# Optimization experiments

Hardware: AMD Instinct MI355X
Metric: run time of the kernel (lower is better)

## Reference

```python
import jax, jax.numpy as jnp
import numpy as np

H, W, C = 96, 96, 21
THETA_ALPHA, THETA_BETA, THETA_GAMMA = 8.0, 0.125, 3.0
NUM_ITERATIONS = 5


def setup_inputs() -> dict:
    key = jax.random.key(0)
    k1, k2, k3, k4, k5 = jax.random.split(key, 5)
    unaries = jax.random.normal(k1, (1, H, W, C), dtype=jnp.float32)
    reference_image = jax.random.uniform(k2, (1, H, W, 3), dtype=jnp.float32)
    # truncated normal(mean=0, std=0.1) as in tf.initializers.truncated_normal
    spatial_ker_weights = 0.1 * jax.random.truncated_normal(k3, -2.0, 2.0, (C,), dtype=jnp.float32)
    bilateral_ker_weights = 0.1 * jax.random.truncated_normal(k4, -2.0, 2.0, (C,), dtype=jnp.float32)
    compatibility_matrix = 0.1 * jax.random.truncated_normal(k5, -2.0, 2.0, (C, C), dtype=jnp.float32)
    return {
        "unaries": unaries,
        "reference_image": reference_image,
        "spatial_ker_weights": spatial_ker_weights,
        "bilateral_ker_weights": bilateral_ker_weights,
        "compatibility_matrix": compatibility_matrix,
    }


def _gaussian_kernel(feats):
    # feats: [B, N, D] -> K[b, i, j] = exp(-0.5 * ||f_i - f_j||^2)
    sq = jnp.sum(feats * feats, axis=-1)  # [B, N]
    d2 = sq[:, :, None] + sq[:, None, :] - 2.0 * jnp.einsum("bnd,bmd->bnm", feats, feats)
    return jnp.exp(-0.5 * jnp.maximum(d2, 0.0))


def _build_kernels(reference_image):
    # Exact-math equivalent of the permutohedral lattice Gaussian filter:
    # spatial features = positions/theta_gamma; bilateral = [pos/theta_alpha, rgb/theta_beta].
    B = reference_image.shape[0]
    yy, xx = jnp.meshgrid(jnp.arange(H, dtype=jnp.float32), jnp.arange(W, dtype=jnp.float32), indexing="ij")
    pos = jnp.stack([yy, xx], axis=-1).reshape(1, H * W, 2)  # [1, N, 2]
    pos = jnp.broadcast_to(pos, (B, H * W, 2))
    col = reference_image.reshape(B, H * W, 3)
    k_spatial = _gaussian_kernel(pos / THETA_GAMMA)
    k_bilateral = _gaussian_kernel(jnp.concatenate([pos / THETA_ALPHA, col / THETA_BETA], axis=-1))
    return k_spatial, k_bilateral


def reference(unaries, reference_image, spatial_ker_weights, bilateral_ker_weights, compatibility_matrix):
    B = unaries.shape[0]
    N = H * W
    k_spatial, k_bilateral = _build_kernels(reference_image)  # built once; reused each iteration
    u = unaries.reshape(B, N, C)
    q = u
    for _ in range(NUM_ITERATIONS):
        q = jax.nn.softmax(q, axis=-1)
        spatial_out = jnp.einsum("bnm,bmc->bnc", k_spatial, q)
        bilateral_out = jnp.einsum("bnm,bmc->bnc", k_bilateral, q)
        # pairwise^T = compat @ diag(w_s) @ S^T + compat @ diag(w_b) @ Bi^T
        # => pairwise = (S * w_s + Bi * w_b) @ compat^T
        message = spatial_out * spatial_ker_weights + bilateral_out * bilateral_ker_weights
        pairwise = message @ compatibility_matrix.T
        q = u - pairwise
    return q.reshape(unaries.shape)
```

## Files before the change

### kernel.cpp

```cpp
#include <hip/hip_runtime.h>
#include <hip/hip_bf16.h>

#define HH 96
#define WW 96
#define CC 21
#define NN (HH*WW)
#define NELEM (NN*CC)
#define RS 20
#define NPAR (2*CC + CC*CC)
#define L2E 1.4426950408889634f
#define NMC 48
#define NBB (36*NMC)
#define NBLUR (CC*8)
#define SROWS 12
#define TRUNC2 900
#define BLURKEY 0x10000

typedef short bf16x8 __attribute__((ext_vector_type(8)));
typedef float f32x16 __attribute__((ext_vector_type(16)));

__device__ __forceinline__ float fexp2(float x) { return __builtin_amdgcn_exp2f(x); }
__device__ __forceinline__ float fexp(float x)  { return __builtin_amdgcn_exp2f(x * L2E); }

__device__ __forceinline__ short f2b(float f) {
    __hip_bfloat16 h = __float2bfloat16(f);
    short s; __builtin_memcpy(&s, &h, 2); return s;
}

struct Tab { int n; int k[NBB + NBLUR]; };
constexpr Tab build_tab() {
    Tab t{};
    int key[NBB + NBLUR] = {};
    int cst[NBB + NBLUR] = {};
    int m = 0;
    for (int nt = 0; nt < 36; nt++)
        for (int mc = 0; mc < NMC; mc++) {
            const int ny0 = (nt / 6) * 16, nx0 = (nt % 6) * 16;
            const int my0 = (mc & 7) * 12, mx0 = (mc >> 3) * 16;
            const int dx = (mx0 > nx0 + 15) ? mx0 - (nx0 + 15)
                         : ((nx0 > mx0 + 15) ? nx0 - (mx0 + 15) : 0);
            const int lim = TRUNC2 - dx * dx;
            if (lim < 0) continue;
            int T = 0;
            while ((T + 1) * (T + 1) <= lim) T++;
            int cost = 0;
            for (int wv = 0; wv < 4; wv++) {
                const int by0 = ny0 + 4 * wv;
                int lo = by0 - T - my0;     if (lo < 0)  lo = 0;
                int hi = by0 + 3 + T - my0; if (hi > 11) hi = 11;
                if (lo <= hi) cost += hi - lo + 1;
            }
            if (cost == 0) continue;
            key[m] = (nt << 6) | mc; cst[m] = cost; m++;
        }
    for (int b = 0; b < NBLUR; b++) { key[m] = BLURKEY + b; cst[m] = 20; m++; }
    for (int c = 48; c >= 1; c--)
        for (int i = 0; i < m; i++)
            if (cst[i] == c) t.k[t.n++] = key[i];
    return t;
}
constexpr Tab TT = build_tab();
__device__ __constant__ Tab c_TT = TT;

__global__ void k_sniff(const unsigned short* __restrict__ u16, int* __restrict__ flag32) {
    __shared__ int sfound;
    if (threadIdx.x == 0) sfound = 0;
    __syncthreads();
    const int base = blockIdx.x * (NELEM/32);
    int found = 0;
    for (int i = base + threadIdx.x; i < base + NELEM/32; i += 256) {
        unsigned v = u16[i];
        if ((v & 0x7F80u) == 0x7F80u) found = 1;
    }
    if (found) sfound = 1;
    __syncthreads();
    if (threadIdx.x == 0) flag32[blockIdx.x] = sfound;
}

__device__ __forceinline__ int rdflag(const int* __restrict__ flag32) {
    int f = 0;
    #pragma unroll
    for (int i = 0; i < 32; i++) f |= flag32[i];
    return f;
}

__global__ __launch_bounds__(256) void k_prep(
    const void* __restrict__ u, const void* __restrict__ img,
    const void* __restrict__ wS, const void* __restrict__ wB,
    const void* __restrict__ compat, const int* __restrict__ flag32,
    float* __restrict__ uf, float* __restrict__ featx, float* __restrict__ par,
    float* __restrict__ bil, __hip_bfloat16* __restrict__ pT)
{
    const int f = rdflag(flag32);
    const int tid = threadIdx.x;
    const int n = blockIdx.x * 256 + tid;

    if (blockIdx.x == 0) {
        for (int i = tid; i < NPAR; i += 256) {
            const void* src; int j;
            if (i < CC)        { src = wS;     j = i; }
            else if (i < 2*CC) { src = wB;     j = i - CC; }
            else               { src = compat; j = i - 2*CC; }
            par[i] = f ? ((const float*)src)[j]
                       : __bfloat162float(((const __hip_bfloat16*)src)[j]);
        }
    }

    {
        float c0, c1, c2;
        if (f) { const float* p = (const float*)img;
                 c0 = p[3*n]; c1 = p[3*n+1]; c2 = p[3*n+2]; }
        else   { const __hip_bfloat16* p = (const __hip_bfloat16*)img;
                 c0 = __bfloat162float(p[3*n]); c1 = __bfloat162float(p[3*n+1]);
                 c2 = __bfloat162float(p[3*n+2]); }
        float ym = (float)(n / WW), xm = (float)(n % WW);
        const float sc = 0.15014029f;
        const float cf = 9.6089787f;
        featx[8*n + 0] = -L2E * (fmaf(ym, ym, xm*xm) * 0.0078125f
                                 + 32.f * (c0*c0 + c1*c1 + c2*c2));
        featx[8*n + 1] = sc * ym;
        featx[8*n + 2] = sc * xm;
        featx[8*n + 3] = cf * c0;
        featx[8*n + 4] = cf * c1;
        featx[8*n + 5] = cf * c2;
        featx[8*n + 6] = 0.f;
        featx[8*n + 7] = 0.f;
    }

    float v[CC];
    float mx = -1e30f;
    #pragma unroll
    for (int c = 0; c < CC; c++) {
        float uv = f ? ((const float*)u)[n*CC + c]
                     : __bfloat162float(((const __hip_bfloat16*)u)[n*CC + c]);
        uf[n*CC + c] = uv;
        v[c] = uv;
        mx = fmaxf(mx, uv);
    }
    float s = 0.f;
    #pragma unroll
    for (int c = 0; c < CC; c++) { v[c] = fexp(v[c] - mx); s += v[c]; }
    float inv = 1.f / s;
    #pragma unroll
    for (int c = 0; c < CC; c++) {
        pT[(size_t)c*NN + n] = __float2bfloat16(v[c] * inv);
        bil[(size_t)c*NN + n] = 0.f;
    }
}

__global__ __launch_bounds__(256, 4) void k_work(
    const __hip_bfloat16* __restrict__ pT,
    const float* __restrict__ featx,
    float* __restrict__ bil,
    float* __restrict__ s2T)
{
    __shared__ float smem[6176];
    const int tid = threadIdx.x;
    const int item = c_TT.k[blockIdx.x];

    if (item < BLURKEY) {
        float* lds_h = smem;
        const int wv   = tid >> 6, lane = tid & 63;
        const int quad = lane >> 5, lid = lane & 31;

        const int nt = item >> 6, mc = item & 63;
        const int ny0 = (nt / 6) * 16, nx0 = (nt % 6) * 16;
        const int my0 = (mc & 7) * 12, mx0 = (mc >> 3) * 16;

        const int dx = (mx0 > nx0 + 15) ? mx0 - (nx0 + 15)
                     : ((nx0 > mx0 + 15) ? nx0 - (mx0 + 15) : 0);
        const int lim = TRUNC2 - dx * dx;
        int T = (int)sqrtf((float)lim);
        T -= (T * T > lim);
        T += ((T + 1) * (T + 1) <= lim);

        int blo = ny0 - T - my0;      blo = blo < 0 ? 0 : blo;
        int bhi = ny0 + 15 + T - my0; bhi = bhi > 11 ? 11 : bhi;

        {
            float4* dst = (float4*)lds_h;
            for (int i = blo * 32 + tid; i < (bhi + 1) * 32; i += 256) {
                const int seg = i >> 5, off = i & 31;
                dst[i] = ((const float4*)(featx +
                          (size_t)((my0 + seg) * WW + mx0) * 8))[off];
            }
        }
        __syncthreads();

        const int by0 = ny0 + 4 * wv;
        int lo = by0 - T - my0;     lo = lo < 0 ? 0 : lo;
        int hi = by0 + 3 + T - my0; hi = hi > 11 ? 11 : hi;
        if (lo > hi) return;

        const int row = lid >> 4, col = lid & 15;
        const int n0 = (by0 + row) * WW + nx0 + col;
        const int n1 = n0 + 2 * WW;
        const float4 g0a = *(const float4*)(featx + (size_t)n0 * 8);
        const float4 g0b = *(const float4*)(featx + (size_t)n0 * 8 + 4);
        const float4 g1a = *(const float4*)(featx + (size_t)n1 * 8);
        const float4 g1b = *(const float4*)(featx + (size_t)n1 * 8 + 4);

        f32x16 acc0, acc1;
        #pragma unroll
        for (int r = 0; r < 16; r++) { acc0[r] = 0.f; acc1[r] = 0.f; }

        int mg = (my0 + lo) * WW + mx0 + quad * 8;
        for (int step = lo; step <= hi; step++, mg += WW) {
            bf16x8 afrag = *(const bf16x8*)(pT + (size_t)lid * NN + mg);

            const float* h = lds_h + (step * 16 + quad * 8) * 8;
            float kb0[8], kb1[8];
            #pragma unroll
            for (int j = 0; j < 8; j++) {
                float4 ha = *(const float4*)(h + j * 8);
                float4 hb = *(const float4*)(h + j * 8 + 4);
                float s0 = g0a.x + ha.x;
                s0 = fmaf(g0a.y, ha.y, s0);
                s0 = fmaf(g0a.z, ha.z, s0);
                s0 = fmaf(g0a.w, ha.w, s0);
                s0 = fmaf(g0b.x, hb.x, s0);
                s0 = fmaf(g0b.y, hb.y, s0);
                kb0[j] = fexp2(s0);
                float s1 = g1a.x + ha.x;
                s1 = fmaf(g1a.y, ha.y, s1);
                s1 = fmaf(g1a.z, ha.z, s1);
                s1 = fmaf(g1a.w, ha.w, s1);
                s1 = fmaf(g1b.x, hb.x, s1);
                s1 = fmaf(g1b.y, hb.y, s1);
                kb1[j] = fexp2(s1);
            }
            bf16x8 b0, b1;
            #pragma unroll
            for (int j = 0; j < 8; j++) { b0[j] = f2b(kb0[j]); b1[j] = f2b(kb1[j]); }

            acc0 = __builtin_amdgcn_mfma_f32_32x32x16_bf16(afrag, b0, acc0, 0, 0, 0);
            acc1 = __builtin_amdgcn_mfma_f32_32x32x16_bf16(afrag, b1, acc1, 0, 0, 0);
        }

        #pragma unroll
        for (int r = 0; r < 16; r++) {
            int c = (r & 3) + 8 * (r >> 2) + 4 * quad;
            if (c < CC) {
                atomicAdd(&bil[(size_t)c * NN + n0], acc0[r]);
                atomicAdd(&bil[(size_t)c * NN + n1], acc1[r]);
            }
        }
    } else {
        float* A   = smem;
        float* B2  = smem + 4992;
        float* w_s = smem + 6144;
        const int b2 = item - BLURKEY;
        const int c = b2 % CC;
        const int strip = b2 / CC;
        const int y0 = strip * SROWS;
        const int ylo = (y0 - RS < 0) ? 0 : y0 - RS;
        const int yhi = (y0 + SROWS - 1 + RS > HH - 1) ? HH - 1 : y0 + SROWS - 1 + RS;
        const int nrows = yhi - ylo + 1;

        if (tid <= RS) w_s[tid] = fexp2(-(float)(tid*tid) * (L2E / 18.f));
        const __hip_bfloat16* src = pT + (size_t)c * NN + ylo * WW;
        for (int i = tid; i < nrows * WW; i += 256)
            A[i] = __bfloat162float(src[i]);
        __syncthreads();

        for (int i = tid; i < SROWS * WW; i += 256) {
            const int yo = y0 + i / WW;
            const int x  = i % WW;
            float acc = A[(yo - ylo) * WW + x];
            #pragma unroll
            for (int d = 1; d <= RS; d++) {
                float s = 0.f;
                if (yo - d >= 0)  s += A[(yo - d - ylo) * WW + x];
                if (yo + d < HH)  s += A[(yo + d - ylo) * WW + x];
                acc = fmaf(w_s[d], s, acc);
            }
            B2[i] = acc;
        }
        __syncthreads();

        for (int i = tid; i < SROWS * WW; i += 256) {
            const int r = i / WW, x = i % WW;
            float acc = B2[i];
            #pragma unroll
            for (int d = 1; d <= RS; d++) {
                float s = 0.f;
                if (x - d >= 0)  s += B2[r * WW + x - d];
                if (x + d < WW)  s += B2[r * WW + x + d];
                acc = fmaf(w_s[d], s, acc);
            }
            s2T[(size_t)c * NN + (y0 + r) * WW + x] = acc;
        }
    }
}

__global__ __launch_bounds__(256) void k_update(
    float* __restrict__ bil, const float* __restrict__ s2T,
    const float* __restrict__ uf, const float* __restrict__ par,
    const int* __restrict__ flag32,
    __hip_bfloat16* __restrict__ pT, void* __restrict__ out, int last)
{
    __shared__ float sc[CC*CC + 1];
    __shared__ float sws[CC], swb[CC];
    const int tid = threadIdx.x;
    for (int i = tid; i < CC*CC; i += 256) sc[i] = par[2*CC + i];
    if (tid == 0) sc[CC*CC] = 0.f;
    if (tid < CC) { sws[tid] = par[tid]; swb[tid] = par[CC + tid]; }
    __syncthreads();

    const int half = tid & 1;
    const int n = blockIdx.x * 128 + (tid >> 1);

    float msg[11];
    #pragma unroll
    for (int k = 0; k < 11; k++) {
        const int cp = 2*k + half;
        if (cp < CC) {
            msg[k] = fmaf(s2T[(size_t)cp*NN + n], sws[cp],
                          bil[(size_t)cp*NN + n] * swb[cp]);
            bil[(size_t)cp*NN + n] = 0.f;
        } else msg[k] = 0.f;
    }

    float pw[CC];
    #pragma unroll
    for (int c = 0; c < CC; c++) {
        float a = msg[0] * sc[c*CC + half];
        #pragma unroll
        for (int k = 1; k < 11; k++)
            a = fmaf(msg[k], sc[c*CC + 2*k + half], a);
        pw[c] = a;
    }
    #pragma unroll
    for (int c = 0; c < CC; c++)
        pw[c] += __shfl_xor(pw[c], 1, 64);

    float qv[CC];
    float mx = -1e30f;
    #pragma unroll
    for (int c = 0; c < CC; c++) {
        qv[c] = uf[(size_t)n*CC + c] - pw[c];
        mx = fmaxf(mx, qv[c]);
    }

    if (last) {
        const int is_f32 = rdflag(flag32);
        #pragma unroll
        for (int k = 0; k < 11; k++) {
            const int ce = 2*k, co = (k < 10) ? 2*k + 1 : 0;
            float v = half ? qv[co] : qv[ce];
            const int c = 2*k + half;
            if (c < CC) {
                if (is_f32) ((float*)out)[(size_t)n*CC + c] = v;
                else ((__hip_bfloat16*)out)[(size_t)n*CC + c] = __float2bfloat16(v);
            }
        }
    } else {
        float ex[11]; float ssum = 0.f;
        #pragma unroll
        for (int k = 0; k < 11; k++) {
            const int ce = 2*k, co = (k < 10) ? 2*k + 1 : 0;
            float v = half ? qv[co] : qv[ce];
            float e = fexp(v - mx);
            if (2*k + half < CC) ssum += e;
            ex[k] = e;
        }
        ssum += __shfl_xor(ssum, 1, 64);
        const float inv = 1.f / ssum;
        #pragma unroll
        for (int k = 0; k < 11; k++) {
            const int c = 2*k + half;
            if (c < CC) pT[(size_t)c*NN + n] = __float2bfloat16(ex[k] * inv);
        }
    }
}

extern "C" void kernel_launch(void* const* d_in, const int* in_sizes, int n_in,
                              void* d_out, int out_size, void* d_ws, size_t ws_size,
                              hipStream_t stream)
{
    float* ws = (float*)d_ws;
    int*   flag32 = (int*)ws;
    float* par    = ws + 32;
    float* featx  = ws + 544;
    __hip_bfloat16* pT = (__hip_bfloat16*)(ws + 74272);
    float* uf  = ws + 221728;
    float* s2T = uf + NELEM;
    float* bil = s2T + NELEM;

    k_sniff<<<32, 256, 0, stream>>>((const unsigned short*)d_in[0], flag32);
    k_prep<<<NN/256, 256, 0, stream>>>(d_in[0], d_in[1], d_in[2], d_in[3], d_in[4],
                                       flag32, uf, featx, par, bil, pT);

    for (int it = 0; it < 5; it++) {
        k_work<<<TT.n, 256, 0, stream>>>(pT, featx, bil, s2T);
        k_update<<<NN/128, 256, 0, stream>>>(bil, s2T, uf, par, flag32,
                                             pT, d_out, (it == 4) ? 1 : 0);
    }
}
```

Before: 231.1 us.

## Fuse update into work kernel via per-tile completion counters and double-buffered probabilities

Removes the separate k_update launch. Each work block bumps an atomic counter for the output tile(s) it contributed to, and the block that finishes a tile last runs the compatibility transform, softmax and output write for that tile. Probabilities are double-buffered so the next iteration's values can be written while other blocks still read the current ones. This saves five kernel launches and their tail gaps. In exchange it adds threadfences, atomics and serial tail work in the last-arriving blocks, and drops the occupancy hint from launch_bounds.

Result: slower. 645.9 us (+179.5%).

```diff
diff --git a/kernel.cpp b/kernel.cpp
--- a/kernel.cpp
+++ b/kernel.cpp
@@ -27,12 +27,13 @@
     short s; __builtin_memcpy(&s, &h, 2); return s;
 }
 
-struct Tab { int n; int k[NBB + NBLUR]; };
+struct Tab { int n; int k[NBB + NBLUR]; int expct[36]; };
 constexpr Tab build_tab() {
     Tab t{};
     int key[NBB + NBLUR] = {};
     int cst[NBB + NBLUR] = {};
     int m = 0;
+    for (int nt = 0; nt < 36; nt++) t.expct[nt] = 42;
     for (int nt = 0; nt < 36; nt++)
         for (int mc = 0; mc < NMC; mc++) {
             const int ny0 = (nt / 6) * 16, nx0 = (nt % 6) * 16;
@@ -52,6 +53,7 @@
             }
             if (cost == 0) continue;
             key[m] = (nt << 6) | mc; cst[m] = cost; m++;
+            t.expct[nt]++;
         }
     for (int b = 0; b < NBLUR; b++) { key[m] = BLURKEY + b; cst[m] = 20; m++; }
     for (int c = 48; c >= 1; c--)
@@ -89,13 +91,14 @@
     const void* __restrict__ wS, const void* __restrict__ wB,
     const void* __restrict__ compat, const int* __restrict__ flag32,
     float* __restrict__ uf, float* __restrict__ featx, float* __restrict__ par,
-    float* __restrict__ bil, __hip_bfloat16* __restrict__ pT)
+    float* __restrict__ bil, __hip_bfloat16* __restrict__ pT, int* __restrict__ cnt)
 {
     const int f = rdflag(flag32);
     const int tid = threadIdx.x;
     const int n = blockIdx.x * 256 + tid;
 
     if (blockIdx.x == 0) {
+        if (tid < 36) cnt[tid] = 0;
         for (int i = tid; i < NPAR; i += 256) {
             const void* src; int j;
             if (i < CC)        { src = wS;     j = i; }
@@ -148,15 +151,21 @@
     }
 }
 
-__global__ __launch_bounds__(256, 4) void k_work(
-    const __hip_bfloat16* __restrict__ pT,
+__global__ __launch_bounds__(256) void k_work(
+    const __hip_bfloat16* __restrict__ pTcur,
+    __hip_bfloat16* __restrict__ pTnxt,
     const float* __restrict__ featx,
     float* __restrict__ bil,
-    float* __restrict__ s2T)
+    float* __restrict__ s2T,
+    const float* __restrict__ uf, const float* __restrict__ par,
+    const int* __restrict__ flag32, int* __restrict__ cnt,
+    void* __restrict__ out, int last)
 {
     __shared__ float smem[6176];
+    __shared__ int fin[13];
     const int tid = threadIdx.x;
     const int item = c_TT.k[blockIdx.x];
+    if (tid == 0) fin[0] = 0;
 
     if (item < BLURKEY) {
         float* lds_h = smem;
@@ -190,61 +199,70 @@
         const int by0 = ny0 + 4 * wv;
         int lo = by0 - T - my0;     lo = lo < 0 ? 0 : lo;
         int hi = by0 + 3 + T - my0; hi = hi > 11 ? 11 : hi;
-        if (lo > hi) return;
-
-        const int row = lid >> 4, col = lid & 15;
-        const int n0 = (by0 + row) * WW + nx0 + col;
-        const int n1 = n0 + 2 * WW;
-        const float4 g0a = *(const float4*)(featx + (size_t)n0 * 8);
-        const float4 g0b = *(const float4*)(featx + (size_t)n0 * 8 + 4);
-        const float4 g1a = *(const float4*)(featx + (size_t)n1 * 8);
-        const float4 g1b = *(const float4*)(featx + (size_t)n1 * 8 + 4);
-
-        f32x16 acc0, acc1;
-        #pragma unroll
-        for (int r = 0; r < 16; r++) { acc0[r] = 0.f; acc1[r] = 0.f; }
-
-        int mg = (my0 + lo) * WW + mx0 + quad * 8;
-        for (int step = lo; step <= hi; step++, mg += WW) {
-            bf16x8 afrag = *(const bf16x8*)(pT + (size_t)lid * NN + mg);
-
-            const float* h = lds_h + (step * 16 + quad * 8) * 8;
-            float kb0[8], kb1[8];
-            #pragma unroll
-            for (int j = 0; j < 8; j++) {
-                float4 ha = *(const float4*)(h + j * 8);
-                float4 hb = *(const float4*)(h + j * 8 + 4);
-                float s0 = g0a.x + ha.x;
-                s0 = fmaf(g0a.y, ha.y, s0);
-                s0 = fmaf(g0a.z, ha.z, s0);
-                s0 = fmaf(g0a.w, ha.w, s0);
-                s0 = fmaf(g0b.x, hb.x, s0);
-                s0 = fmaf(g0b.y, hb.y, s0);
-                kb0[j] = fexp2(s0);
-                float s1 = g1a.x + ha.x;
-                s1 = fmaf(g1a.y, ha.y, s1);
-                s1 = fmaf(g1a.z, ha.z, s1);
-                s1 = fmaf(g1a.w, ha.w, s1);
-                s1 = fmaf(g1b.x, hb.x, s1);
-                s1 = fmaf(g1b.y, hb.y, s1);
-                kb1[j] = fexp2(s1);
-            }
-            bf16x8 b0, b1;
-            #pragma unroll
-            for (int j = 0; j < 8; j++) { b0[j] = f2b(kb0[j]); b1[j] = f2b(kb1[j]); }
-
-            acc0 = __builtin_amdgcn_mfma_f32_32x32x16_bf16(afrag, b0, acc0, 0, 0, 0);
-            acc1 = __builtin_amdgcn_mfma_f32_32x32x16_bf16(afrag, b1, acc1, 0, 0, 0);
-        }
-
-        #pragma unroll
-        for (int r = 0; r < 16; r++) {
-            int c = (r & 3) + 8 * (r >> 2) + 4 * quad;
-            if (c < CC) {
-                atomicAdd(&bil[(size_t)c * NN + n0], acc0[r]);
-                atomicAdd(&bil[(size_t)c * NN + n1], acc1[r]);
-            }
-        }
+
+        if (lo <= hi) {
+            const int row = lid >> 4, col = lid & 15;
+            const int n0 = (by0 + row) * WW + nx0 + col;
+            const int n1 = n0 + 2 * WW;
+            const float4 g0a = *(const float4*)(featx + (size_t)n0 * 8);
+            const float4 g0b = *(const float4*)(featx + (size_t)n0 * 8 + 4);
+            const float4 g1a = *(const float4*)(featx + (size_t)n1 * 8);
+            const float4 g1b = *(const float4*)(featx + (size_t)n1 * 8 + 4);
+
+            f32x16 acc0, acc1;
+            #pragma unroll
+            for (int r = 0; r < 16; r++) { acc0[r] = 0.f; acc1[r] = 0.f; }
+
+            int mg = (my0 + lo) * WW + mx0 + quad * 8;
+            for (int step = lo; step <= hi; step++, mg += WW) {
+                bf16x8 afrag = *(const bf16x8*)(pTcur + (size_t)lid * NN + mg);
+
+                const float* h = lds_h + (step * 16 + quad * 8) * 8;
+                float kb0[8], kb1[8];
+                #pragma unroll
+                for (int j = 0; j < 8; j++) {
+                    float4 ha = *(const float4*)(h + j * 8);
+                    float4 hb = *(const float4*)(h + j * 8 + 4);
+                    float s0 = g0a.x + ha.x;
+                    s0 = fmaf(g0a.y, ha.y, s0);
+                    s0 = fmaf(g0a.z, ha.z, s0);
+                    s0 = fmaf(g0a.w, ha.w, s0);
+                    s0 = fmaf(g0b.x, hb.x, s0);
+                    s0 = fmaf(g0b.y, hb.y, s0);
+                    kb0[j] = fexp2(s0);
+                    float s1 = g1a.x + ha.x;
+                    s1 = fmaf(g1a.y, ha.y, s1);
+                    s1 = fmaf(g1a.z, ha.z, s1);
+                    s1 = fmaf(g1a.w, ha.w, s1);
+                    s1 = fmaf(g1b.x, hb.x, s1);
+                    s1 = fmaf(g1b.y, hb.y, s1);
+                    kb1[j] = fexp2(s1);
+                }
+                bf16x8 b0, b1;
+                #pragma unroll
+                for (int j = 0; j < 8; j++) { b0[j] = f2b(kb0[j]); b1[j] = f2b(kb1[j]); }
+
+                acc0 = __builtin_amdgcn_mfma_f32_32x32x16_bf16(afrag, b0, acc0, 0, 0, 0);
+                acc1 = __builtin_amdgcn_mfma_f32_32x32x16_bf16(afrag, b1, acc1, 0, 0, 0);
+            }
+
+            #pragma unroll
+            for (int r = 0; r < 16; r++) {
+                int c = (r & 3) + 8 * (r >> 2) + 4 * quad;
+                if (c < CC) {
+                    atomicAdd(&bil[(size_t)c * NN + n0], acc0[r]);
+                    atomicAdd(&bil[(size_t)c * NN + n1], acc1[r]);
+                }
+            }
+        }
+
+        __threadfence();
+        __syncthreads();
+        if (tid == 0) {
+            int old = atomicAdd(&cnt[nt], 1);
+            if (old == c_TT.expct[nt] - 1) { fin[0] = 1; fin[1] = nt; }
+        }
+        __syncthreads();
     } else {
         float* A   = smem;
         float* B2  = smem + 4992;
@@ -258,7 +276,7 @@
         const int nrows = yhi - ylo + 1;
 
         if (tid <= RS) w_s[tid] = fexp2(-(float)(tid*tid) * (L2E / 18.f));
-        const __hip_bfloat16* src = pT + (size_t)c * NN + ylo * WW;
+        const __hip_bfloat16* src = pTcur + (size_t)c * NN + ylo * WW;
         for (int i = tid; i < nrows * WW; i += 256)
             A[i] = __bfloat162float(src[i]);
         __syncthreads();
@@ -290,87 +308,76 @@
             }
             s2T[(size_t)c * NN + (y0 + r) * WW + x] = acc;
         }
-    }
-}
-
-__global__ __launch_bounds__(256) void k_update(
-    float* __restrict__ bil, const float* __restrict__ s2T,
-    const float* __restrict__ uf, const float* __restrict__ par,
-    const int* __restrict__ flag32,
-    __hip_bfloat16* __restrict__ pT, void* __restrict__ out, int last)
-{
-    __shared__ float sc[CC*CC + 1];
-    __shared__ float sws[CC], swb[CC];
-    const int tid = threadIdx.x;
+
+        __threadfence();
+        __syncthreads();
+        if (tid == 0) {
+            int nf = 0;
+            const int r0 = (12 * strip) / 16;
+            int r1 = (12 * strip + 11) / 16; if (r1 > 5) r1 = 5;
+            for (int r = r0; r <= r1; r++)
+                for (int xt = 0; xt < 6; xt++) {
+                    const int nt2 = r * 6 + xt;
+                    int old = atomicAdd(&cnt[nt2], 1);
+                    if (old == c_TT.expct[nt2] - 1) fin[1 + nf++] = nt2;
+                }
+            fin[0] = nf;
+        }
+        __syncthreads();
+    }
+
+    const int nf = fin[0];
+    if (nf == 0) return;
+    __threadfence();
+
+    float* sc  = smem;
+    float* sws = smem + 448;
+    float* swb = smem + 480;
     for (int i = tid; i < CC*CC; i += 256) sc[i] = par[2*CC + i];
-    if (tid == 0) sc[CC*CC] = 0.f;
     if (tid < CC) { sws[tid] = par[tid]; swb[tid] = par[CC + tid]; }
     __syncthreads();
 
-    const int half = tid & 1;
-    const int n = blockIdx.x * 128 + (tid >> 1);
-
-    float msg[11];
-    #pragma unroll
-    for (int k = 0; k < 11; k++) {
-        const int cp = 2*k + half;
-        if (cp < CC) {
-            msg[k] = fmaf(s2T[(size_t)cp*NN + n], sws[cp],
-                          bil[(size_t)cp*NN + n] * swb[cp]);
-            bil[(size_t)cp*NN + n] = 0.f;
-        } else msg[k] = 0.f;
-    }
-
-    float pw[CC];
-    #pragma unroll
-    for (int c = 0; c < CC; c++) {
-        float a = msg[0] * sc[c*CC + half];
+    const int is_f32 = last ? rdflag(flag32) : 0;
+
+    for (int t = 0; t < nf; t++) {
+        const int nt2 = fin[1 + t];
+        const int n = ((nt2 / 6) * 16 + (tid >> 4)) * WW + (nt2 % 6) * 16 + (tid & 15);
+
+        float msg[CC];
         #pragma unroll
-        for (int k = 1; k < 11; k++)
-            a = fmaf(msg[k], sc[c*CC + 2*k + half], a);
-        pw[c] = a;
-    }
-    #pragma unroll
-    for (int c = 0; c < CC; c++)
-        pw[c] += __shfl_xor(pw[c], 1, 64);
-
-    float qv[CC];
-    float mx = -1e30f;
-    #pragma unroll
-    for (int c = 0; c < CC; c++) {
-        qv[c] = uf[(size_t)n*CC + c] - pw[c];
-        mx = fmaxf(mx, qv[c]);
-    }
-
-    if (last) {
-        const int is_f32 = rdflag(flag32);
+        for (int c = 0; c < CC; c++) {
+            msg[c] = fmaf(s2T[(size_t)c*NN + n], sws[c],
+                          bil[(size_t)c*NN + n] * swb[c]);
+            bil[(size_t)c*NN + n] = 0.f;
+        }
+
+        float qv[CC];
+        float mx = -1e30f;
         #pragma unroll
-        for (int k = 0; k < 11; k++) {
-            const int ce = 2*k, co = (k < 10) ? 2*k + 1 : 0;
-            float v = half ? qv[co] : qv[ce];
-            const int c = 2*k + half;
-            if (c < CC) {
-                if (is_f32) ((float*)out)[(size_t)n*CC + c] = v;
-                else ((__hip_bfloat16*)out)[(size_t)n*CC + c] = __float2bfloat16(v);
-            }
-        }
-    } else {
-        float ex[11]; float ssum = 0.f;
-        #pragma unroll
-        for (int k = 0; k < 11; k++) {
-            const int ce = 2*k, co = (k < 10) ? 2*k + 1 : 0;
-            float v = half ? qv[co] : qv[ce];
-            float e = fexp(v - mx);
-            if (2*k + half < CC) ssum += e;
-            ex[k] = e;
-        }
-        ssum += __shfl_xor(ssum, 1, 64);
-        const float inv = 1.f / ssum;
-        #pragma unroll
-        for (int k = 0; k < 11; k++) {
-            const int c = 2*k + half;
-            if (c < CC) pT[(size_t)c*NN + n] = __float2bfloat16(ex[k] * inv);
-        }
+        for (int c = 0; c < CC; c++) {
+            float pw = 0.f;
+            #pragma unroll
+            for (int cp = 0; cp < CC; cp++) pw = fmaf(msg[cp], sc[c*CC + cp], pw);
+            qv[c] = uf[(size_t)n*CC + c] - pw;
+            mx = fmaxf(mx, qv[c]);
+        }
+
+        if (last) {
+            #pragma unroll
+            for (int c = 0; c < CC; c++) {
+                if (is_f32) ((float*)out)[(size_t)n*CC + c] = qv[c];
+                else ((__hip_bfloat16*)out)[(size_t)n*CC + c] = __float2bfloat16(qv[c]);
+            }
+        } else {
+            float s = 0.f;
+            #pragma unroll
+            for (int c = 0; c < CC; c++) { qv[c] = fexp(qv[c] - mx); s += qv[c]; }
+            float inv = 1.f / s;
+            #pragma unroll
+            for (int c = 0; c < CC; c++)
+                pTnxt[(size_t)c*NN + n] = __float2bfloat16(qv[c] * inv);
+        }
+        if (tid == 0) cnt[nt2] = 0;
     }
 }
 
@@ -382,18 +389,21 @@
     int*   flag32 = (int*)ws;
     float* par    = ws + 32;
     float* featx  = ws + 544;
-    __hip_bfloat16* pT = (__hip_bfloat16*)(ws + 74272);
-    float* uf  = ws + 221728;
+    __hip_bfloat16* pT0 = (__hip_bfloat16*)(ws + 74272);
+    __hip_bfloat16* pT1 = (__hip_bfloat16*)(ws + 221728);
+    float* uf  = ws + 369184;
     float* s2T = uf + NELEM;
     float* bil = s2T + NELEM;
+    int*   cnt = (int*)(bil + NELEM);
 
     k_sniff<<<32, 256, 0, stream>>>((const unsigned short*)d_in[0], flag32);
     k_prep<<<NN/256, 256, 0, stream>>>(d_in[0], d_in[1], d_in[2], d_in[3], d_in[4],
-                                       flag32, uf, featx, par, bil, pT);
+                                       flag32, uf, featx, par, bil, pT0, cnt);
 
     for (int it = 0; it < 5; it++) {
-        k_work<<<TT.n, 256, 0, stream>>>(pT, featx, bil, s2T);
-        k_update<<<NN/128, 256, 0, stream>>>(bil, s2T, uf, par, flag32,
-                                             pT, d_out, (it == 4) ? 1 : 0);
-    }
-}
+        __hip_bfloat16* cur = (it & 1) ? pT1 : pT0;
+        __hip_bfloat16* nxt = (it & 1) ? pT0 : pT1;
+        k_work<<<TT.n, 256, 0, stream>>>(cur, nxt, featx, bil, s2T, uf, par,
+                                         flag32, cnt, d_out, (it == 4) ? 1 : 0);
+    }
+}
```

## Compute bilateral kernel exponent via split-bf16 MFMA instead of scalar FMAs

Applied to the files above, without the earlier changes.

Moves the per-pair dot product of bilateral features from scalar FMA chains onto MFMA instructions. Features are split into bf16 hi/lo pairs to keep accuracy, and the exp'd results are repacked with cross-half shuffles into B fragments for the P^T·K MFMA. The block's feature strip is staged into LDS as bf16 hi/lo, processing two rows per step. It also drops the occupancy hint from launch_bounds. The trade is extra MFMAs, shuffles and register pressure, plus some precision loss from the bf16 split, in exchange for fewer VALU ops.

New measurement: 235.6 us. About the same (+2.0%).

```diff
diff --git a/kernel.cpp b/kernel.cpp
--- a/kernel.cpp
+++ b/kernel.cpp
@@ -18,6 +18,7 @@
 
 typedef short bf16x8 __attribute__((ext_vector_type(8)));
 typedef float f32x16 __attribute__((ext_vector_type(16)));
+typedef int   i32x4  __attribute__((ext_vector_type(4)));
 
 __device__ __forceinline__ float fexp2(float x) { return __builtin_amdgcn_exp2f(x); }
 __device__ __forceinline__ float fexp(float x)  { return __builtin_amdgcn_exp2f(x * L2E); }
@@ -25,6 +26,10 @@
 __device__ __forceinline__ short f2b(float f) {
     __hip_bfloat16 h = __float2bfloat16(f);
     short s; __builtin_memcpy(&s, &h, 2); return s;
+}
+__device__ __forceinline__ float b2f(short s) {
+    __hip_bfloat16 h; __builtin_memcpy(&h, &s, 2);
+    return __bfloat162float(h);
 }
 
 struct Tab { int n; int k[NBB + NBLUR]; };
@@ -148,7 +153,7 @@
     }
 }
 
-__global__ __launch_bounds__(256, 4) void k_work(
+__global__ __launch_bounds__(256) void k_work(
     const __hip_bfloat16* __restrict__ pT,
     const float* __restrict__ featx,
     float* __restrict__ bil,
@@ -159,7 +164,7 @@
     const int item = c_TT.k[blockIdx.x];
 
     if (item < BLURKEY) {
-        float* lds_h = smem;
+        short* hs = (short*)smem;
         const int wv   = tid >> 6, lane = tid & 63;
         const int quad = lane >> 5, lid = lane & 31;
 
@@ -174,15 +179,18 @@
         T -= (T * T > lim);
         T += ((T + 1) * (T + 1) <= lim);
 
-        int blo = ny0 - T - my0;      blo = blo < 0 ? 0 : blo;
-        int bhi = ny0 + 15 + T - my0; bhi = bhi > 11 ? 11 : bhi;
-
-        {
-            float4* dst = (float4*)lds_h;
-            for (int i = blo * 32 + tid; i < (bhi + 1) * 32; i += 256) {
-                const int seg = i >> 5, off = i & 31;
-                dst[i] = ((const float4*)(featx +
-                          (size_t)((my0 + seg) * WW + mx0) * 8))[off];
+        for (int i = tid; i < 192; i += 256) {
+            const int mrow = i >> 4, mcol = i & 15;
+            const float* f = featx + (size_t)((my0 + mrow) * WW + mx0 + mcol) * 8;
+            const int grp = mrow >> 1;
+            const int li  = ((mrow & 1) << 4) | mcol;
+            short* dhi = hs + grp * 512 + li * 8;
+            float hv[8] = {1.f, f[0], f[1], f[2], f[3], f[4], f[5], 0.f};
+            #pragma unroll
+            for (int j = 0; j < 8; j++) {
+                short hb = f2b(hv[j]);
+                dhi[j] = hb;
+                dhi[256 + j] = f2b(hv[j] - b2f(hb));
             }
         }
         __syncthreads();
@@ -195,46 +203,82 @@
         const int row = lid >> 4, col = lid & 15;
         const int n0 = (by0 + row) * WW + nx0 + col;
         const int n1 = n0 + 2 * WW;
-        const float4 g0a = *(const float4*)(featx + (size_t)n0 * 8);
-        const float4 g0b = *(const float4*)(featx + (size_t)n0 * 8 + 4);
-        const float4 g1a = *(const float4*)(featx + (size_t)n1 * 8);
-        const float4 g1b = *(const float4*)(featx + (size_t)n1 * 8 + 4);
-
-        f32x16 acc0, acc1;
-        #pragma unroll
-        for (int r = 0; r < 16; r++) { acc0[r] = 0.f; acc1[r] = 0.f; }
-
-        int mg = (my0 + lo) * WW + mx0 + quad * 8;
-        for (int step = lo; step <= hi; step++, mg += WW) {
-            bf16x8 afrag = *(const bf16x8*)(pT + (size_t)lid * NN + mg);
-
-            const float* h = lds_h + (step * 16 + quad * 8) * 8;
-            float kb0[8], kb1[8];
+
+        bf16x8 gh0, gl0, gh1, gl1;
+        {
+            const float* f0 = featx + (size_t)n0 * 8;
+            const float* f1 = featx + (size_t)n1 * 8;
+            float g0v[8] = {f0[0], 1.f, f0[1], f0[2], f0[3], f0[4], f0[5], 0.f};
+            float g1v[8] = {f1[0], 1.f, f1[1], f1[2], f1[3], f1[4], f1[5], 0.f};
             #pragma unroll
             for (int j = 0; j < 8; j++) {
-                float4 ha = *(const float4*)(h + j * 8);
-                float4 hb = *(const float4*)(h + j * 8 + 4);
-                float s0 = g0a.x + ha.x;
-                s0 = fmaf(g0a.y, ha.y, s0);
-                s0 = fmaf(g0a.z, ha.z, s0);
-                s0 = fmaf(g0a.w, ha.w, s0);
-                s0 = fmaf(g0b.x, hb.x, s0);
-                s0 = fmaf(g0b.y, hb.y, s0);
-                kb0[j] = fexp2(s0);
-                float s1 = g1a.x + ha.x;
-                s1 = fmaf(g1a.y, ha.y, s1);
-                s1 = fmaf(g1a.z, ha.z, s1);
-                s1 = fmaf(g1a.w, ha.w, s1);
-                s1 = fmaf(g1b.x, hb.x, s1);
-                s1 = fmaf(g1b.y, hb.y, s1);
-                kb1[j] = fexp2(s1);
-            }
-            bf16x8 b0, b1;
-            #pragma unroll
-            for (int j = 0; j < 8; j++) { b0[j] = f2b(kb0[j]); b1[j] = f2b(kb1[j]); }
-
-            acc0 = __builtin_amdgcn_mfma_f32_32x32x16_bf16(afrag, b0, acc0, 0, 0, 0);
-            acc1 = __builtin_amdgcn_mfma_f32_32x32x16_bf16(afrag, b1, acc1, 0, 0, 0);
+                short h0b = f2b(g0v[j]); gh0[j] = h0b;
+                gl0[j] = f2b(g0v[j] - b2f(h0b));
+                short h1b = f2b(g1v[j]); gh1[j] = h1b;
+                gl1[j] = f2b(g1v[j] - b2f(h1b));
+            }
+        }
+
+        f32x16 acc0, acc1, zz;
+        #pragma unroll
+        for (int r = 0; r < 16; r++) { acc0[r] = 0.f; acc1[r] = 0.f; zz[r] = 0.f; }
+
+        const int glo2 = lo >> 1, ghi2 = hi >> 1;
+        for (int g = glo2; g <= ghi2; g++) {
+            bf16x8 A1 = *(const bf16x8*)(hs + g * 512 + quad * 256 + lid * 8);
+            const int mrow = my0 + 2 * g;
+            const __hip_bfloat16* pbase = pT + (size_t)lid * NN + mrow * WW + mx0 + quad * 8;
+            bf16x8 afA = *(const bf16x8*)(pbase);
+            bf16x8 afB = *(const bf16x8*)(pbase + WW);
+
+            {
+                f32x16 V = __builtin_amdgcn_mfma_f32_32x32x16_bf16(A1, gh0, zz, 0, 0, 0);
+                V = __builtin_amdgcn_mfma_f32_32x32x16_bf16(A1, gl0, V, 0, 0, 0);
+                #pragma unroll
+                for (int r = 0; r < 16; r++) V[r] = fexp2(V[r]);
+                int P[8];
+                #pragma unroll
+                for (int t2 = 0; t2 < 8; t2++)
+                    P[t2] = (int)(((unsigned)(unsigned short)f2b(V[2*t2]))
+                          | (((unsigned)(unsigned short)f2b(V[2*t2+1])) << 16));
+                int S0 = __shfl_xor(P[0], 32), S1 = __shfl_xor(P[1], 32);
+                int S2 = __shfl_xor(P[2], 32), S3 = __shfl_xor(P[3], 32);
+                int S4 = __shfl_xor(P[4], 32), S5 = __shfl_xor(P[5], 32);
+                int S6 = __shfl_xor(P[6], 32), S7 = __shfl_xor(P[7], 32);
+                i32x4 b1i = { quad ? S2 : P[0], quad ? S3 : P[1],
+                              quad ? P[2] : S0, quad ? P[3] : S1 };
+                i32x4 b2i = { quad ? S6 : P[4], quad ? S7 : P[5],
+                              quad ? P[6] : S4, quad ? P[7] : S5 };
+                bf16x8 b1, b2;
+                __builtin_memcpy(&b1, &b1i, 16);
+                __builtin_memcpy(&b2, &b2i, 16);
+                acc0 = __builtin_amdgcn_mfma_f32_32x32x16_bf16(afA, b1, acc0, 0, 0, 0);
+                acc0 = __builtin_amdgcn_mfma_f32_32x32x16_bf16(afB, b2, acc0, 0, 0, 0);
+            }
+            {
+                f32x16 V = __builtin_amdgcn_mfma_f32_32x32x16_bf16(A1, gh1, zz, 0, 0, 0);
+                V = __builtin_amdgcn_mfma_f32_32x32x16_bf16(A1, gl1, V, 0, 0, 0);
+                #pragma unroll
+                for (int r = 0; r < 16; r++) V[r] = fexp2(V[r]);
+                int P[8];
+                #pragma unroll
+                for (int t2 = 0; t2 < 8; t2++)
+                    P[t2] = (int)(((unsigned)(unsigned short)f2b(V[2*t2]))
+                          | (((unsigned)(unsigned short)f2b(V[2*t2+1])) << 16));
+                int S0 = __shfl_xor(P[0], 32), S1 = __shfl_xor(P[1], 32);
+                int S2 = __shfl_xor(P[2], 32), S3 = __shfl_xor(P[3], 32);
+                int S4 = __shfl_xor(P[4], 32), S5 = __shfl_xor(P[5], 32);
+                int S6 = __shfl_xor(P[6], 32), S7 = __shfl_xor(P[7], 32);
+                i32x4 b1i = { quad ? S2 : P[0], quad ? S3 : P[1],
+                              quad ? P[2] : S0, quad ? P[3] : S1 };
+                i32x4 b2i = { quad ? S6 : P[4], quad ? S7 : P[5],
+                              quad ? P[6] : S4, quad ? P[7] : S5 };
+                bf16x8 b1, b2;
+                __builtin_memcpy(&b1, &b1i, 16);
+                __builtin_memcpy(&b2, &b2i, 16);
+                acc1 = __builtin_amdgcn_mfma_f32_32x32x16_bf16(afA, b1, acc1, 0, 0, 0);
+                acc1 = __builtin_amdgcn_mfma_f32_32x32x16_bf16(afB, b2, acc1, 0, 0, 0);
+            }
         }
 
         #pragma unroll
```

## Spread bilateral atomics across 8 slot buffers and tighten truncation radius

Applied to the files above, without the earlier changes.

The bilateral accumulation, previously atomic adds into a single buffer, now goes to one of eight slot copies chosen by block index, which cuts atomic contention. The update kernel sums the eight slots and zeroes them, and now runs with smaller blocks (128 threads, 64 pixels) so there are more of them. The squared-distance truncation also drops from 900 to 729, which prunes more tile pairs from the work table. The cost is eight times the memory traffic for reading and zeroing the bilateral buffer, plus a slightly coarser approximation of the Gaussian kernel.

Result: slower. 245.4 us (+6.2%).

```diff
diff --git a/kernel.cpp b/kernel.cpp
--- a/kernel.cpp
+++ b/kernel.cpp
@@ -13,8 +13,9 @@
 #define NBB (36*NMC)
 #define NBLUR (CC*8)
 #define SROWS 12
-#define TRUNC2 900
+#define TRUNC2 729
 #define BLURKEY 0x10000
+#define NSLOT 8
 
 typedef short bf16x8 __attribute__((ext_vector_type(8)));
 typedef float f32x16 __attribute__((ext_vector_type(16)));
@@ -89,7 +90,7 @@
     const void* __restrict__ wS, const void* __restrict__ wB,
     const void* __restrict__ compat, const int* __restrict__ flag32,
     float* __restrict__ uf, float* __restrict__ featx, float* __restrict__ par,
-    float* __restrict__ bil, __hip_bfloat16* __restrict__ pT)
+    float* __restrict__ bil8, __hip_bfloat16* __restrict__ pT)
 {
     const int f = rdflag(flag32);
     const int tid = threadIdx.x;
@@ -144,14 +145,16 @@
     #pragma unroll
     for (int c = 0; c < CC; c++) {
         pT[(size_t)c*NN + n] = __float2bfloat16(v[c] * inv);
-        bil[(size_t)c*NN + n] = 0.f;
+        #pragma unroll
+        for (int sl = 0; sl < NSLOT; sl++)
+            bil8[((size_t)sl*CC + c)*NN + n] = 0.f;
     }
 }
 
 __global__ __launch_bounds__(256, 4) void k_work(
     const __hip_bfloat16* __restrict__ pT,
     const float* __restrict__ featx,
-    float* __restrict__ bil,
+    float* __restrict__ bil8,
     float* __restrict__ s2T)
 {
     __shared__ float smem[6176];
@@ -237,12 +240,13 @@
             acc1 = __builtin_amdgcn_mfma_f32_32x32x16_bf16(afrag, b1, acc1, 0, 0, 0);
         }
 
+        float* dst = bil8 + (size_t)(blockIdx.x & (NSLOT - 1)) * CC * NN;
         #pragma unroll
         for (int r = 0; r < 16; r++) {
             int c = (r & 3) + 8 * (r >> 2) + 4 * quad;
             if (c < CC) {
-                atomicAdd(&bil[(size_t)c * NN + n0], acc0[r]);
-                atomicAdd(&bil[(size_t)c * NN + n1], acc1[r]);
+                atomicAdd(&dst[(size_t)c * NN + n0], acc0[r]);
+                atomicAdd(&dst[(size_t)c * NN + n1], acc1[r]);
             }
         }
     } else {
@@ -293,8 +297,8 @@
     }
 }
 
-__global__ __launch_bounds__(256) void k_update(
-    float* __restrict__ bil, const float* __restrict__ s2T,
+__global__ __launch_bounds__(128) void k_update(
+    float* __restrict__ bil8, const float* __restrict__ s2T,
     const float* __restrict__ uf, const float* __restrict__ par,
     const int* __restrict__ flag32,
     __hip_bfloat16* __restrict__ pT, void* __restrict__ out, int last)
@@ -302,22 +306,32 @@
     __shared__ float sc[CC*CC + 1];
     __shared__ float sws[CC], swb[CC];
     const int tid = threadIdx.x;
-    for (int i = tid; i < CC*CC; i += 256) sc[i] = par[2*CC + i];
+    for (int i = tid; i < CC*CC; i += 128) sc[i] = par[2*CC + i];
     if (tid == 0) sc[CC*CC] = 0.f;
     if (tid < CC) { sws[tid] = par[tid]; swb[tid] = par[CC + tid]; }
     __syncthreads();
 
     const int half = tid & 1;
-    const int n = blockIdx.x * 128 + (tid >> 1);
+    const int n = blockIdx.x * 64 + (tid >> 1);
 
     float msg[11];
     #pragma unroll
     for (int k = 0; k < 11; k++) {
         const int cp = 2*k + half;
         if (cp < CC) {
-            msg[k] = fmaf(s2T[(size_t)cp*NN + n], sws[cp],
-                          bil[(size_t)cp*NN + n] * swb[cp]);
-            bil[(size_t)cp*NN + n] = 0.f;
+            float b0 = bil8[((size_t)(0*CC + cp))*NN + n];
+            float b1 = bil8[((size_t)(1*CC + cp))*NN + n];
+            float b2 = bil8[((size_t)(2*CC + cp))*NN + n];
+            float b3 = bil8[((size_t)(3*CC + cp))*NN + n];
+            float b4 = bil8[((size_t)(4*CC + cp))*NN + n];
+            float b5 = bil8[((size_t)(5*CC + cp))*NN + n];
+            float b6 = bil8[((size_t)(6*CC + cp))*NN + n];
+            float b7 = bil8[((size_t)(7*CC + cp))*NN + n];
+            float b = ((b0 + b1) + (b2 + b3)) + ((b4 + b5) + (b6 + b7));
+            msg[k] = fmaf(s2T[(size_t)cp*NN + n], sws[cp], b * swb[cp]);
+            #pragma unroll
+            for (int sl = 0; sl < NSLOT; sl++)
+                bil8[((size_t)sl*CC + cp)*NN + n] = 0.f;
         } else msg[k] = 0.f;
     }
 
@@ -383,17 +397,17 @@
     float* par    = ws + 32;
     float* featx  = ws + 544;
     __hip_bfloat16* pT = (__hip_bfloat16*)(ws + 74272);
-    float* uf  = ws + 221728;
-    float* s2T = uf + NELEM;
-    float* bil = s2T + NELEM;
+    float* uf   = ws + 221728;
+    float* s2T  = uf + NELEM;
+    float* bil8 = s2T + NELEM;
 
     k_sniff<<<32, 256, 0, stream>>>((const unsigned short*)d_in[0], flag32);
     k_prep<<<NN/256, 256, 0, stream>>>(d_in[0], d_in[1], d_in[2], d_in[3], d_in[4],
-                                       flag32, uf, featx, par, bil, pT);
+                                       flag32, uf, featx, par, bil8, pT);
 
     for (int it = 0; it < 5; it++) {
-        k_work<<<TT.n, 256, 0, stream>>>(pT, featx, bil, s2T);
-        k_update<<<NN/128, 256, 0, stream>>>(bil, s2T, uf, par, flag32,
-                                             pT, d_out, (it == 4) ? 1 : 0);
-    }
-}
+        k_work<<<TT.n, 256, 0, stream>>>(pT, featx, bil8, s2T);
+        k_update<<<NN/64, 128, 0, stream>>>(bil8, s2T, uf, par, flag32,
+                                            pT, d_out, (it == 4) ? 1 : 0);
+    }
+}
```
